# Kernel tuning notes

Measured on AMD Instinct MI355X. Metric: run time of the kernel, lower is better.

Reference implementation:

```python
import jax, jax.numpy as jnp
import numpy as np

TEMPERATURE = 8.0  # init arg


def setup_inputs() -> dict:
    key = jax.random.key(0)
    kq, kv, kk = jax.random.split(key, 3)
    B, W, H, C, M, D = 4, 64, 64, 256, 32, 32
    q = jax.random.normal(kq, (B, W, H, M, D), dtype=jnp.float32)
    v = jax.random.normal(kv, (B, W, H, C, M), dtype=jnp.float32)
    k = jax.random.normal(kk, (B, W, H, D, 1), dtype=jnp.float32)
    return {"q": q, "v": v, "k": k}


def reference(q, v, k):
    # attn = (q / T) @ k : [B,W,H,M,1]
    attn = jnp.matmul(q / TEMPERATURE, k)
    # softmax over dim=-2 (the query/slot axis M), NOT the usual key axis
    attn = jax.nn.softmax(attn, axis=-2)
    # v @ attn : [B,W,H,C,M] @ [B,W,H,M,1] -> [B,W,H,C,1] -> squeeze -> [B,W,H,C]
    out = jnp.matmul(v, attn)[..., 0]
    # permute(0,3,1,2) -> [B,C,W,H]; the subsequent .view is a no-op reshape
    return jnp.transpose(out, (0, 3, 1, 2))
```

## Files before the change

### kernel.cpp

```cpp
#include <hip/hip_runtime.h>


#define TEMP_INV 0.125f

__global__ __launch_bounds__(256) void sdpa_kernel(
    const float* __restrict__ q,
    const float* __restrict__ v,
    const float* __restrict__ k,
    float* __restrict__ out)
{
    const int p = blockIdx.x;
    const int t = threadIdx.x;
    const int b  = p >> 12;
    const int wh = p & 4095;

    __shared__ float s_k[32];
    __shared__ float s_logit[32];
    __shared__ float s_attn[32];

    if (t < 32) s_k[t] = k[p * 32 + t] * TEMP_INV;
    __syncthreads();

    const int j = t & 7;
    {
        const float4 q4 = ((const float4*)q)[p * 256 + t];
        float partial = q4.x * s_k[j * 4 + 0] + q4.y * s_k[j * 4 + 1]
                      + q4.z * s_k[j * 4 + 2] + q4.w * s_k[j * 4 + 3];
        partial += __shfl_down(partial, 4, 8);
        partial += __shfl_down(partial, 2, 8);
        partial += __shfl_down(partial, 1, 8);
        if (j == 0) s_logit[t >> 3] = partial;
    }
    __syncthreads();

    if (t < 32) {
        float l = s_logit[t];
        float mx = l;
        #pragma unroll
        for (int off = 16; off; off >>= 1)
            mx = fmaxf(mx, __shfl_xor(mx, off, 32));
        float e = __expf(l - mx);
        float sum = e;
        #pragma unroll
        for (int off = 16; off; off >>= 1)
            sum += __shfl_xor(sum, off, 32);
        s_attn[t] = e / sum;
    }
    __syncthreads();

    const float a0 = s_attn[j * 4 + 0];
    const float a1 = s_attn[j * 4 + 1];
    const float a2 = s_attn[j * 4 + 2];
    const float a3 = s_attn[j * 4 + 3];

    const float4* v4p = (const float4*)v + (size_t)p * 2048;
    float acc[8];
    #pragma unroll
    for (int i = 0; i < 8; ++i) {
        const float4 v4 = v4p[t + 256 * i];
        acc[i] = v4.x * a0 + v4.y * a1 + v4.z * a2 + v4.w * a3;
    }
    #pragma unroll
    for (int i = 0; i < 8; ++i) {
        acc[i] += __shfl_down(acc[i], 4, 8);
        acc[i] += __shfl_down(acc[i], 2, 8);
        acc[i] += __shfl_down(acc[i], 1, 8);
    }
    if (j == 0) {
        const int c0 = t >> 3;
        #pragma unroll
        for (int i = 0; i < 8; ++i) {
            out[(b * 256 + (c0 + 32 * i)) * 4096 + wh] = acc[i];
        }
    }
}

extern "C" void kernel_launch(void* const* d_in, const int* in_sizes, int n_in,
                              void* d_out, int out_size, void* d_ws, size_t ws_size,
                              hipStream_t stream) {
    const float* q = (const float*)d_in[0];
    const float* v = (const float*)d_in[1];
    const float* k = (const float*)d_in[2];
    float* out = (float*)d_out;
    sdpa_kernel<<<16384, 256, 0, stream>>>(q, v, k, out);
}
```

Measured before the change: 725.3 us.

## Batch 16 positions per block and stage output in LDS for coalesced writes

Each block now handles 16 consecutive (w,h) positions instead of one. Results go into a padded shared-memory tile and are then written as float4 runs along the contiguous wh axis of the transposed output. This replaces the strided scalar stores with wider coalesced stores and amortizes the k loads. The cost is fewer blocks (1024), which risks lower occupancy and less memory-level parallelism for streaming v.

```diff
diff --git a/kernel.cpp b/kernel.cpp
--- a/kernel.cpp
+++ b/kernel.cpp
@@ -2,6 +2,7 @@
 
 
 #define TEMP_INV 0.125f
+#define G 16
 
 __global__ __launch_bounds__(256) void sdpa_kernel(
     const float* __restrict__ q,
@@ -9,68 +10,92 @@
     const float* __restrict__ k,
     float* __restrict__ out)
 {
-    const int p = blockIdx.x;
-    const int t = threadIdx.x;
-    const int b  = p >> 12;
-    const int wh = p & 4095;
+    const int t   = threadIdx.x;
+    const int p0  = blockIdx.x * G;
+    const int b   = p0 >> 12;
+    const int wh0 = p0 & 4095;
 
-    __shared__ float s_k[32];
-    __shared__ float s_logit[32];
-    __shared__ float s_attn[32];
+    __shared__ float s_k[G * 32];
+    __shared__ float s_logit[G * 32];
+    __shared__ float s_attn[G * 32];
+    __shared__ float s_out[256 * 17];
 
-    if (t < 32) s_k[t] = k[p * 32 + t] * TEMP_INV;
+    if (t < 128) {
+        float4 k4 = ((const float4*)k)[p0 * 8 + t];
+        k4.x *= TEMP_INV; k4.y *= TEMP_INV; k4.z *= TEMP_INV; k4.w *= TEMP_INV;
+        ((float4*)s_k)[t] = k4;
+    }
     __syncthreads();
 
     const int j = t & 7;
-    {
-        const float4 q4 = ((const float4*)q)[p * 256 + t];
-        float partial = q4.x * s_k[j * 4 + 0] + q4.y * s_k[j * 4 + 1]
-                      + q4.z * s_k[j * 4 + 2] + q4.w * s_k[j * 4 + 3];
+    const int m = t >> 3;
+    #pragma unroll 2
+    for (int g = 0; g < G; ++g) {
+        const float4 q4 = ((const float4*)q)[(p0 + g) * 256 + t];
+        const float* kg = &s_k[g * 32 + j * 4];
+        float partial = q4.x * kg[0] + q4.y * kg[1] + q4.z * kg[2] + q4.w * kg[3];
         partial += __shfl_down(partial, 4, 8);
         partial += __shfl_down(partial, 2, 8);
         partial += __shfl_down(partial, 1, 8);
-        if (j == 0) s_logit[t >> 3] = partial;
+        if (j == 0) s_logit[g * 32 + m] = partial;
     }
     __syncthreads();
 
-    if (t < 32) {
-        float l = s_logit[t];
-        float mx = l;
+    {
+        const int mm = t & 31;
         #pragma unroll
-        for (int off = 16; off; off >>= 1)
-            mx = fmaxf(mx, __shfl_xor(mx, off, 32));
-        float e = __expf(l - mx);
-        float sum = e;
-        #pragma unroll
-        for (int off = 16; off; off >>= 1)
-            sum += __shfl_xor(sum, off, 32);
-        s_attn[t] = e / sum;
+        for (int r = 0; r < 2; ++r) {
+            const int g = (t >> 5) + r * 8;
+            float l = s_logit[g * 32 + mm];
+            float mx = l;
+            #pragma unroll
+            for (int off = 16; off; off >>= 1)
+                mx = fmaxf(mx, __shfl_xor(mx, off, 32));
+            float e = __expf(l - mx);
+            float s = e;
+            #pragma unroll
+            for (int off = 16; off; off >>= 1)
+                s += __shfl_xor(s, off, 32);
+            s_attn[g * 32 + mm] = e / s;
+        }
     }
     __syncthreads();
 
-    const float a0 = s_attn[j * 4 + 0];
-    const float a1 = s_attn[j * 4 + 1];
-    const float a2 = s_attn[j * 4 + 2];
-    const float a3 = s_attn[j * 4 + 3];
-
-    const float4* v4p = (const float4*)v + (size_t)p * 2048;
-    float acc[8];
-    #pragma unroll
-    for (int i = 0; i < 8; ++i) {
-        const float4 v4 = v4p[t + 256 * i];
-        acc[i] = v4.x * a0 + v4.y * a1 + v4.z * a2 + v4.w * a3;
-    }
-    #pragma unroll
-    for (int i = 0; i < 8; ++i) {
-        acc[i] += __shfl_down(acc[i], 4, 8);
-        acc[i] += __shfl_down(acc[i], 2, 8);
-        acc[i] += __shfl_down(acc[i], 1, 8);
-    }
-    if (j == 0) {
-        const int c0 = t >> 3;
+    const int c0 = t >> 3;
+    #pragma unroll 2
+    for (int g = 0; g < G; ++g) {
+        const float* ag = &s_attn[g * 32 + j * 4];
+        const float a0 = ag[0], a1 = ag[1], a2 = ag[2], a3 = ag[3];
+        const float4* v4p = (const float4*)v + (size_t)(p0 + g) * 2048;
+        float acc[8];
         #pragma unroll
         for (int i = 0; i < 8; ++i) {
-            out[(b * 256 + (c0 + 32 * i)) * 4096 + wh] = acc[i];
+            const float4 v4 = v4p[t + 256 * i];
+            acc[i] = v4.x * a0 + v4.y * a1 + v4.z * a2 + v4.w * a3;
+        }
+        #pragma unroll
+        for (int i = 0; i < 8; ++i) {
+            acc[i] += __shfl_down(acc[i], 4, 8);
+            acc[i] += __shfl_down(acc[i], 2, 8);
+            acc[i] += __shfl_down(acc[i], 1, 8);
+        }
+        if (j == 0) {
+            #pragma unroll
+            for (int i = 0; i < 8; ++i)
+                s_out[(c0 + 32 * i) * 17 + g] = acc[i];
+        }
+    }
+    __syncthreads();
+
+    {
+        const int c  = t >> 2;
+        const int gc = t & 3;
+        #pragma unroll
+        for (int i = 0; i < 4; ++i) {
+            const int cc = c + 64 * i;
+            const float* so = &s_out[cc * 17 + gc * 4];
+            const float4 o4 = make_float4(so[0], so[1], so[2], so[3]);
+            ((float4*)out)[(size_t)(b * 256 + cc) * 1024 + (wh0 >> 2) + gc] = o4;
         }
     }
 }
@@ -82,5 +107,5 @@
     const float* v = (const float*)d_in[1];
     const float* k = (const float*)d_in[2];
     float* out = (float*)d_out;
-    sdpa_kernel<<<16384, 256, 0, stream>>>(q, v, k, out);
+    sdpa_kernel<<<16384 / G, 256, 0, stream>>>(q, v, k, out);
 }
```

After: 717.6 us. About the same (-1.1%).
